# Optimization experiments

Hardware: AMD Instinct MI355X
Metric: run time of the kernel (lower is better)

The kernel has to match this reference:

```python
import jax, jax.numpy as jnp
import numpy as np

B, F = 8192, 256
H1, H2, H3 = 32, 64, 32
ORDER = 2
OUT = 1


def setup_inputs() -> dict:
    key = jax.random.key(0)
    ks = jax.random.split(key, 6)
    x = jax.random.normal(ks[0], (B, F), dtype=jnp.float32)
    # stacked per-feature FeatureNet weights, fan-in scaled to keep ReLUs active
    W1 = jax.random.normal(ks[1], (F, 1, H1), dtype=jnp.float32) * 1.0
    b1 = jnp.zeros((F, H1), dtype=jnp.float32)
    W2 = jax.random.normal(ks[2], (F, H1, H2), dtype=jnp.float32) * (1.0 / np.sqrt(H1))
    b2 = jnp.zeros((F, H2), dtype=jnp.float32)
    W3 = jax.random.normal(ks[3], (F, H2, H3), dtype=jnp.float32) * (1.0 / np.sqrt(H2))
    b3 = jnp.zeros((F, H3), dtype=jnp.float32)
    Wout = jax.random.normal(ks[4], (ORDER * H3, OUT), dtype=jnp.float32) * (1.0 / np.sqrt(ORDER * H3))
    bout = jnp.zeros((OUT,), dtype=jnp.float32)
    return {"x": x, "W1": W1, "b1": b1, "W2": W2, "b2": b2,
            "W3": W3, "b3": b3, "Wout": Wout, "bout": bout}


def _feature_nets(x, W1, b1, W2, b2, W3, b3):
    # x: [B, F] -> per-feature tiny MLP 1->32->64->32, batched over F
    h = jax.nn.relu(x[:, :, None] * W1[:, 0, :][None] + b1[None])      # [B, F, 32]
    h = jax.nn.relu(jnp.einsum('bfh,fho->bfo', h, W2) + b2[None])       # [B, F, 64]
    h = jax.nn.relu(jnp.einsum('bfh,fho->bfo', h, W3) + b3[None])       # [B, F, 32]
    return h


def reference(x, W1, b1, W2, b2, W3, b3, Wout, bout):
    t = _feature_nets(x, W1, b1, W2, b2, W3, b3)  # [B, F, H3]
    # Newton's identity power-sum recurrence over interaction order
    p1 = t.sum(axis=1)                            # [B, H3]
    powers = [None, p1]                           # powers[0] unused (scalar 1 in orig)
    inters = [jnp.ones_like(p1), p1]              # interactions[0] = 1 (broadcast)
    for i in range(2, ORDER + 1):
        powers.append(jnp.power(t, i).sum(axis=1))
        cur = 0.0
        for j in range(1, i + 1):
            cur = cur + ((-1.0) ** (j + 1)) * powers[j] * inters[i - j]
        inters.append(cur / i)
    feats = jnp.concatenate(inters[1:], axis=1)   # [B, ORDER*H3]
    pred = feats @ Wout + bout                    # [B, OUT]
    return pred
```

## Files before the change

kernel.cpp:

```cpp
#include <hip/hip_runtime.h>
#include <hip/hip_bf16.h>

#define B_   8192
#define F_   256
#define NFC  16
#define NF   (F_/NFC)
#define NPH  (NF/2)
#define RPB  128
#define NSUB 2

typedef __attribute__((ext_vector_type(8))) short v8s;
typedef __attribute__((ext_vector_type(4))) float v4f;
typedef __attribute__((ext_vector_type(4))) unsigned int v4u;

static __device__ __forceinline__ unsigned short f2bf(float f) {
    __hip_bfloat16 h = __float2bfloat16(f);
    return __builtin_bit_cast(unsigned short, h);
}

static __device__ __forceinline__ unsigned cvtpk(float a, float b) {
    unsigned r;
    asm("v_cvt_pk_bf16_f32 %0, %1, %2" : "=v"(r) : "v"(a), "v"(b));
    return r;
}

static __device__ __forceinline__ void gload_lds16(const void* g, void* l) {
    __builtin_amdgcn_global_load_lds(
        (const __attribute__((address_space(1))) unsigned int*)g,
        (__attribute__((address_space(3))) unsigned int*)l,
        16, 0, 0);
}

__global__ __launch_bounds__(256)
void honam_prep(const float* __restrict__ w2g, const float* __restrict__ w3g,
                const float* __restrict__ w1g, const float* __restrict__ b1g,
                const float* __restrict__ b2g, const float* __restrict__ b3g,
                unsigned short* __restrict__ wf, float* __restrict__ pp)
{
    const int f   = blockIdx.x;
    const int tid = threadIdx.x;
    const float* w2 = w2g + (size_t)f * 2048;
    const float* w3 = w3g + (size_t)f * 2048;
    unsigned short* dst = wf + (size_t)f * 4096;
    for (int i = tid; i < 4096; i += 256) {
        const int frag = i >> 9;
        const int l    = (i >> 3) & 63;
        const int j    = i & 7;
        const int c    = l & 15;
        const int g    = l >> 4;
        float v;
        if (frag < 4) {
            v = w2[(g * 8 + j) * 64 + frag * 16 + c];
        } else {
            const int kk = (frag - 4) >> 1;
            const int n2 = (frag - 4) & 1;
            const int u  = (kk * 2 + (j >> 2)) * 16 + g * 4 + (j & 3);
            v = w3[u * 32 + n2 * 16 + c];
        }
        dst[i] = f2bf(v);
    }
    if (tid < 160) {
        float v;
        if (tid < 32)       v = w1g[f * 32 + tid];
        else if (tid < 64)  v = b1g[f * 32 + (tid - 32)];
        else if (tid < 128) v = b2g[f * 64 + (tid - 64)];
        else                v = b3g[f * 32 + (tid - 128)];
        pp[(size_t)f * 160 + tid] = v;
    }
}

__global__ __launch_bounds__(256, 3)
void honam_k1(const float* __restrict__ xg,
              const unsigned short* __restrict__ wfg, const float* __restrict__ ppg,
              float* __restrict__ p1part, float* __restrict__ p2part)
{
    __shared__ float xs[NF][RPB];
    __shared__ float ps[NF * 160];
    __shared__ short wbuf[2][2][4096] __attribute__((aligned(16)));

    const int tid  = threadIdx.x;
    const int wave = tid >> 6;
    const int lane = tid & 63;
    const int c16  = lane & 15;
    const int g4   = lane >> 4;

    const int bx = blockIdx.x;
    const int rb = bx >> 4;
    const int fc = bx & 15;
    const int r0 = rb * RPB;
    const int f0 = fc * NF;

    {
        const int row  = tid >> 1;
        const int half = tid & 1;
        const float4 va = *(const float4*)&xg[(size_t)(r0 + row) * F_ + f0 + half * 8];
        const float4 vb = *(const float4*)&xg[(size_t)(r0 + row) * F_ + f0 + half * 8 + 4];
        const int fb = half * 8;
        xs[fb + 0][row] = va.x; xs[fb + 1][row] = va.y;
        xs[fb + 2][row] = va.z; xs[fb + 3][row] = va.w;
        xs[fb + 4][row] = vb.x; xs[fb + 5][row] = vb.y;
        xs[fb + 6][row] = vb.z; xs[fb + 7][row] = vb.w;
    }
    {
        const float4* src = (const float4*)(ppg + (size_t)f0 * 160);
        float4* dst = (float4*)ps;
        dst[tid]       = src[tid];
        dst[tid + 256] = src[tid + 256];
        if (tid < 128) dst[tid + 512] = src[tid + 512];
    }

    auto stage = [&](int set, int fp, int fl) {
        const char* src = (const char*)wfg + (size_t)(f0 + fl) * 8192
                        + (2 * wave) * 1024 + lane * 16;
        gload_lds16(src,        &wbuf[set][fp][(2 * wave) * 512]);
        gload_lds16(src + 1024, &wbuf[set][fp][(2 * wave + 1) * 512]);
    };

    stage(0, 0, 0);
    stage(0, 1, 1);
    __syncthreads();

    float2 pacc1[NSUB][2][2];
    float2 pacc2[NSUB][2][2];
#pragma unroll
    for (int s = 0; s < NSUB; ++s)
#pragma unroll
        for (int n2 = 0; n2 < 2; ++n2)
#pragma unroll
            for (int jp = 0; jp < 2; ++jp) {
                pacc1[s][n2][jp] = make_float2(0.f, 0.f);
                pacc2[s][n2][jp] = make_float2(0.f, 0.f);
            }

    auto computeFeat = [&](int set, int fp, int fl) {
        const short* wb = &wbuf[set][fp][0];
        v8s wfr[8];
#pragma unroll
        for (int fr = 0; fr < 8; ++fr)
            wfr[fr] = *(const v8s*)&wb[fr * 512 + lane * 8];

        const int fb = fl * 160;
        const float4 w1a = *(const float4*)&ps[fb + g4 * 8];
        const float4 w1b = *(const float4*)&ps[fb + g4 * 8 + 4];
        const float4 b1a = *(const float4*)&ps[fb + 32 + g4 * 8];
        const float4 b1b = *(const float4*)&ps[fb + 32 + g4 * 8 + 4];
        const float w1v[8] = {w1a.x, w1a.y, w1a.z, w1a.w, w1b.x, w1b.y, w1b.z, w1b.w};
        const float b1v[8] = {b1a.x, b1a.y, b1a.z, b1a.w, b1b.x, b1b.y, b1b.z, b1b.w};
        float b3v[2];
#pragma unroll
        for (int n = 0; n < 2; ++n) b3v[n] = ps[fb + 128 + n * 16 + c16];

        float xm[NSUB];
#pragma unroll
        for (int s = 0; s < NSUB; ++s)
            xm[s] = xs[fl][s * 64 + wave * 16 + c16];

#pragma unroll
        for (int sub = 0; sub < NSUB; ++sub) {
            unsigned h1p[4];
#pragma unroll
            for (int jj = 0; jj < 4; ++jj) {
                const float e0 = fmaxf(fmaf(xm[sub], w1v[2 * jj],     b1v[2 * jj]),     0.f);
                const float e1 = fmaxf(fmaf(xm[sub], w1v[2 * jj + 1], b1v[2 * jj + 1]), 0.f);
                h1p[jj] = cvtpk(e0, e1);
            }
            const v8s bh1 = __builtin_bit_cast(v8s, (v4u){h1p[0], h1p[1], h1p[2], h1p[3]});

            v4f acc2[4];
#pragma unroll
            for (int n = 0; n < 4; ++n) {
                const v4f b2cv = *(const v4f*)&ps[fb + 64 + n * 16 + g4 * 4];
                acc2[n] = __builtin_amdgcn_mfma_f32_16x16x32_bf16(wfr[n], bh1, b2cv, 0, 0, 0);
            }

            unsigned q[8];
#pragma unroll
            for (int n = 0; n < 4; ++n) {
                q[2 * n]     = cvtpk(fmaxf(acc2[n][0], 0.f), fmaxf(acc2[n][1], 0.f));
                q[2 * n + 1] = cvtpk(fmaxf(acc2[n][2], 0.f), fmaxf(acc2[n][3], 0.f));
            }
            const v8s a2k0 = __builtin_bit_cast(v8s, (v4u){q[0], q[1], q[2], q[3]});
            const v8s a2k1 = __builtin_bit_cast(v8s, (v4u){q[4], q[5], q[6], q[7]});

            v4f acc3[2];
#pragma unroll
            for (int n2 = 0; n2 < 2; ++n2) {
                acc3[n2] = __builtin_amdgcn_mfma_f32_16x16x32_bf16(
                    a2k0, wfr[4 + n2], (v4f){b3v[n2], b3v[n2], b3v[n2], b3v[n2]}, 0, 0, 0);
                acc3[n2] = __builtin_amdgcn_mfma_f32_16x16x32_bf16(
                    a2k1, wfr[6 + n2], acc3[n2], 0, 0, 0);
            }
#pragma unroll
            for (int n2 = 0; n2 < 2; ++n2)
#pragma unroll
                for (int jp = 0; jp < 2; ++jp) {
                    float2 t;
                    t.x = fmaxf(acc3[n2][2 * jp],     0.f);
                    t.y = fmaxf(acc3[n2][2 * jp + 1], 0.f);
                    pacc1[sub][n2][jp].x += t.x;
                    pacc1[sub][n2][jp].y += t.y;
                    pacc2[sub][n2][jp].x += t.x * t.x;
                    pacc2[sub][n2][jp].y += t.y * t.y;
                }
        }
    };

#pragma unroll 2
    for (int ph = 0; ph < NPH; ++ph) {
        const int set = ph & 1;
        if (ph + 1 < NPH) {
            stage(set ^ 1, 0, 2 * ph + 2);
            stage(set ^ 1, 1, 2 * ph + 3);
        }
        computeFeat(set, 0, 2 * ph);
        computeFeat(set, 1, 2 * ph + 1);
        __syncthreads();
    }

    float* p1c = p1part + (size_t)fc * (B_ * 32);
    float* p2c = p2part + (size_t)fc * (B_ * 32);
#pragma unroll
    for (int sub = 0; sub < NSUB; ++sub)
#pragma unroll
        for (int n2 = 0; n2 < 2; ++n2)
#pragma unroll
            for (int jp = 0; jp < 2; ++jp) {
                const int row = r0 + sub * 64 + wave * 16 + g4 * 4 + 2 * jp;
                const int col = n2 * 16 + c16;
                p1c[row * 32 + col]       = pacc1[sub][n2][jp].x;
                p1c[(row + 1) * 32 + col] = pacc1[sub][n2][jp].y;
                p2c[row * 32 + col]       = pacc2[sub][n2][jp].x;
                p2c[(row + 1) * 32 + col] = pacc2[sub][n2][jp].y;
            }
}

__global__ __launch_bounds__(256)
void honam_k2(const float* __restrict__ p1part, const float* __restrict__ p2part,
              const float* __restrict__ woutg, const float* __restrict__ boutg,
              float* __restrict__ outg)
{
    const int tid = threadIdx.x;
    const int o   = tid & 31;
    const int r   = blockIdx.x * 8 + (tid >> 5);
    const size_t idx = (size_t)r * 32 + o;

    float s1 = 0.f, s2 = 0.f;
#pragma unroll
    for (int fc = 0; fc < NFC; ++fc) {
        s1 += p1part[(size_t)fc * (B_ * 32) + idx];
        s2 += p2part[(size_t)fc * (B_ * 32) + idx];
    }
    const float wa = woutg[o];
    const float wb = woutg[32 + o];
    float val = s1 * wa + 0.5f * (s1 * s1 - s2) * wb;
#pragma unroll
    for (int off = 16; off > 0; off >>= 1)
        val += __shfl_down(val, off, 32);
    if (o == 0) outg[r] = val + boutg[0];
}

extern "C" void kernel_launch(void* const* d_in, const int* in_sizes, int n_in,
                              void* d_out, int out_size, void* d_ws, size_t ws_size,
                              hipStream_t stream)
{
    const float* xg    = (const float*)d_in[0];
    const float* w1g   = (const float*)d_in[1];
    const float* b1g   = (const float*)d_in[2];
    const float* w2g   = (const float*)d_in[3];
    const float* b2g   = (const float*)d_in[4];
    const float* w3g   = (const float*)d_in[5];
    const float* b3g   = (const float*)d_in[6];
    const float* woutg = (const float*)d_in[7];
    const float* boutg = (const float*)d_in[8];
    float* outg = (float*)d_out;

    float* p1part = (float*)d_ws;
    float* p2part = p1part + (size_t)NFC * B_ * 32;
    unsigned short* wf = (unsigned short*)(p2part + (size_t)NFC * B_ * 32);
    float* pp = (float*)(wf + (size_t)F_ * 4096);

    honam_prep<<<dim3(F_), dim3(256), 0, stream>>>(w2g, w3g, w1g, b1g, b2g, b3g, wf, pp);

    honam_k1<<<dim3((B_ / RPB) * NFC), dim3(256), 0, stream>>>(
        xg, wf, pp, p1part, p2part);

    honam_k2<<<dim3(B_ / 8), dim3(256), 0, stream>>>(p1part, p2part, woutg, boutg, outg);
}
```

Before: 50.13 us.

## Load MFMA weight fragments directly into registers with register double-buffering

```diff
diff --git a/kernel.cpp b/kernel.cpp
--- a/kernel.cpp
+++ b/kernel.cpp
@@ -5,7 +5,6 @@
 #define F_   256
 #define NFC  16
 #define NF   (F_/NFC)
-#define NPH  (NF/2)
 #define RPB  128
 #define NSUB 2
 
@@ -22,13 +21,6 @@
     unsigned r;
     asm("v_cvt_pk_bf16_f32 %0, %1, %2" : "=v"(r) : "v"(a), "v"(b));
     return r;
-}
-
-static __device__ __forceinline__ void gload_lds16(const void* g, void* l) {
-    __builtin_amdgcn_global_load_lds(
-        (const __attribute__((address_space(1))) unsigned int*)g,
-        (__attribute__((address_space(3))) unsigned int*)l,
-        16, 0, 0);
 }
 
 __global__ __launch_bounds__(256)
@@ -69,14 +61,13 @@
     }
 }
 
-__global__ __launch_bounds__(256, 3)
+__global__ __launch_bounds__(256, 4)
 void honam_k1(const float* __restrict__ xg,
               const unsigned short* __restrict__ wfg, const float* __restrict__ ppg,
               float* __restrict__ p1part, float* __restrict__ p2part)
 {
     __shared__ float xs[NF][RPB];
     __shared__ float ps[NF * 160];
-    __shared__ short wbuf[2][2][4096] __attribute__((aligned(16)));
 
     const int tid  = threadIdx.x;
     const int wave = tid >> 6;
@@ -108,16 +99,6 @@
         dst[tid + 256] = src[tid + 256];
         if (tid < 128) dst[tid + 512] = src[tid + 512];
     }
-
-    auto stage = [&](int set, int fp, int fl) {
-        const char* src = (const char*)wfg + (size_t)(f0 + fl) * 8192
-                        + (2 * wave) * 1024 + lane * 16;
-        gload_lds16(src,        &wbuf[set][fp][(2 * wave) * 512]);
-        gload_lds16(src + 1024, &wbuf[set][fp][(2 * wave + 1) * 512]);
-    };
-
-    stage(0, 0, 0);
-    stage(0, 1, 1);
     __syncthreads();
 
     float2 pacc1[NSUB][2][2];
@@ -132,13 +113,14 @@
                 pacc2[s][n2][jp] = make_float2(0.f, 0.f);
             }
 
-    auto computeFeat = [&](int set, int fp, int fl) {
-        const short* wb = &wbuf[set][fp][0];
-        v8s wfr[8];
-#pragma unroll
-        for (int fr = 0; fr < 8; ++fr)
-            wfr[fr] = *(const v8s*)&wb[fr * 512 + lane * 8];
-
+    const char* wlane = (const char*)wfg + (size_t)f0 * 8192 + (size_t)lane * 16;
+
+    v8s wcur[8], wnxt[8];
+#pragma unroll
+    for (int fr = 0; fr < 8; ++fr)
+        wcur[fr] = *(const v8s*)(wlane + fr * 1024);
+
+    auto computeFeat = [&](const v8s* wfr, int fl) {
         const int fb = fl * 160;
         const float4 w1a = *(const float4*)&ps[fb + g4 * 8];
         const float4 w1b = *(const float4*)&ps[fb + g4 * 8 + 4];
@@ -206,15 +188,16 @@
     };
 
 #pragma unroll 2
-    for (int ph = 0; ph < NPH; ++ph) {
-        const int set = ph & 1;
-        if (ph + 1 < NPH) {
-            stage(set ^ 1, 0, 2 * ph + 2);
-            stage(set ^ 1, 1, 2 * ph + 3);
+    for (int fi = 0; fi < NF; ++fi) {
+        if (fi + 1 < NF) {
+            const char* wn = wlane + (size_t)(fi + 1) * 8192;
+#pragma unroll
+            for (int fr = 0; fr < 8; ++fr)
+                wnxt[fr] = *(const v8s*)(wn + fr * 1024);
         }
-        computeFeat(set, 0, 2 * ph);
-        computeFeat(set, 1, 2 * ph + 1);
-        __syncthreads();
+        computeFeat(wcur, fi);
+#pragma unroll
+        for (int fr = 0; fr < 8; ++fr) wcur[fr] = wnxt[fr];
     }
 
     float* p1c = p1part + (size_t)fc * (B_ * 32);
```

Result: slower. 102.4 us (+104.2%).
